# Kernel optimization log

Measured on AMD Instinct MI355X. Metric: run time of the kernel, lower is better.

## Reference

```python
import jax, jax.numpy as jnp
import numpy as np
from jax import lax

B, T, I, O = 32, 4096, 16, 16


def setup_inputs() -> dict:
    key = jax.random.key(0)
    k1, k2, k3, k4 = jax.random.split(key, 4)
    u_in = jax.random.normal(k1, (B, T, I), dtype=jnp.float32)
    # parameters, initialized as in the torch module's __init__
    b_coeff = jax.random.normal(k2, (O, I, 2), dtype=jnp.float32) * 0.01
    rho = jax.random.normal(k3, (O, I, 1), dtype=jnp.float32) * 0.1
    psi = jax.random.normal(k4, (O, I, 1), dtype=jnp.float32) * 0.1
    return {"u_in": u_in, "b_coeff": b_coeff, "rho": rho, "psi": psi}


def _second_order_mimo(u_in, b_coeff, rho, psi):
    # stable parametrization of poles: r = |pole|, theta = angle
    r = jax.nn.sigmoid(rho)[..., 0]            # (O, I)
    theta = np.pi * jax.nn.sigmoid(psi)[..., 0]  # (O, I)
    a1 = -2.0 * r * jnp.cos(theta)             # (O, I)
    a2 = r * r                                  # (O, I)
    b0 = b_coeff[..., 0]                        # (O, I)
    b1 = b_coeff[..., 1]                        # (O, I)

    # FIR (moving-average) part, fully parallel over time:
    # x[b,t,o,i] = b0[o,i]*u[b,t,i] + b1[o,i]*u[b,t-1,i], zero initial condition
    u_prev = jnp.pad(u_in, ((0, 0), (1, 0), (0, 0)))[:, :-1, :]
    x = u_in[:, :, None, :] * b0 + u_prev[:, :, None, :] * b1  # (B, T, O, I)

    # AR (recursive) part: y[t] = x[t] - a1*y[t-1] - a2*y[t-2], per (o,i) pair
    x_t = jnp.moveaxis(x, 1, 0)  # (T, B, O, I)

    def step(carry, xt):
        y1, y2 = carry  # y[t-1], y[t-2], each (B, O, I)
        y = xt - a1 * y1 - a2 * y2
        return (y, y1), y

    y_init = jnp.zeros(x_t.shape[1:], x_t.dtype)
    _, ys = lax.scan(step, (y_init, y_init), x_t)  # (T, B, O, I)

    # sum per-input-channel filter responses -> (B, T, O)
    return jnp.moveaxis(ys.sum(axis=-1), 0, 1)


def reference(u_in, b_coeff, rho, psi):
    return _second_order_mimo(u_in, b_coeff, rho, psi)
```

## Files before the change

kernel.cpp:

```cpp
#include <hip/hip_runtime.h>
#include <math.h>

namespace {

constexpr int B = 32, T = 4096, I = 16, O = 16;

constexpr int C = 128;
constexpr int L = T / C;
constexpr int W = 32;
constexpr int PF = 8;

__device__ __forceinline__ void channel_params(const float* __restrict__ bc,
                                               const float* __restrict__ rho,
                                               const float* __restrict__ psi,
                                               int o, int i,
                                               float& b0, float& b1, float& a1, float& a2) {
    int oi = o * I + i;
    b0 = bc[oi * 2 + 0];
    b1 = bc[oi * 2 + 1];
    float r     = 1.0f / (1.0f + expf(-rho[oi]));
    float theta = 3.14159265358979323846f / (1.0f + expf(-psi[oi]));
    a1 = -2.0f * r * cosf(theta);
    a2 = r * r;
}

template <int NSTEP, int SKIP>
__device__ __forceinline__ void run_chain(const float* __restrict__ up,
        const float b0[4], const float b1[4], const float na1[4], const float na2[4],
        float uprev[4], float* __restrict__ op, bool writer) {
    float y1[4] = {0.f, 0.f, 0.f, 0.f};
    float y2[4] = {0.f, 0.f, 0.f, 0.f};
    float4 buf[PF];
#pragma unroll
    for (int p = 0; p < PF; ++p) buf[p] = *(const float4*)(up + p * I);
#pragma unroll
    for (int t = 0; t < NSTEP; ++t) {
        float4 a = buf[t % PF];
        if (t + PF < NSTEP)
            buf[t % PF] = *(const float4*)(up + (t + PF) * I);
        float uc[4] = {a.x, a.y, a.z, a.w};
        float yv[4];
#pragma unroll
        for (int j = 0; j < 4; ++j) {
            float x = fmaf(b1[j], uprev[j], b0[j] * uc[j]);
            float y = fmaf(na2[j], y2[j], fmaf(na1[j], y1[j], x));
            y2[j] = y1[j]; y1[j] = y; uprev[j] = uc[j];
            yv[j] = y;
        }
        if (t >= SKIP) {
            float s = (yv[0] + yv[1]) + (yv[2] + yv[3]);
            s += __shfl_xor(s, 1);
            s += __shfl_xor(s, 2);
            if (writer) op[(t - SKIP) * O] = s;
        }
    }
}

__global__ __launch_bounds__(256) void mimo_kernel(
        const float* __restrict__ u, const float* __restrict__ bc,
        const float* __restrict__ rho, const float* __restrict__ psi,
        float* __restrict__ out) {
    int g = blockIdx.x * blockDim.x + threadIdx.x;
    int q = g & 3, o = (g >> 2) & 15, b = (g >> 6) & 31, k = g >> 11;
    int i0 = q * 4;

    float b0[4], b1[4], na1[4], na2[4];
#pragma unroll
    for (int j = 0; j < 4; ++j) {
        float B0, B1, A1, A2;
        channel_params(bc, rho, psi, o, i0 + j, B0, B1, A1, A2);
        b0[j] = B0; b1[j] = B1; na1[j] = -A1; na2[j] = -A2;
    }

    int t0 = k * L;
    int start = (k == 0) ? 0 : (t0 - W);
    const float* up = u + ((size_t)b * T + start) * I + i0;

    float uprev[4];
    if (start == 0) {
#pragma unroll
        for (int j = 0; j < 4; ++j) uprev[j] = 0.0f;
    } else {
        float4 r0 = *(const float4*)(up - I);
        uprev[0] = r0.x; uprev[1] = r0.y; uprev[2] = r0.z; uprev[3] = r0.w;
    }

    float* op = out + ((size_t)b * T + t0) * O + o;
    bool writer = (q == 0);

    if (k == 0) run_chain<L, 0>(up, b0, b1, na1, na2, uprev, op, writer);
    else        run_chain<W + L, W>(up, b0, b1, na1, na2, uprev, op, writer);
}

}

extern "C" void kernel_launch(void* const* d_in, const int* in_sizes, int n_in,
                              void* d_out, int out_size, void* d_ws, size_t ws_size,
                              hipStream_t stream) {
    (void)in_sizes; (void)n_in; (void)out_size; (void)d_ws; (void)ws_size;
    const float* u   = (const float*)d_in[0];
    const float* bc  = (const float*)d_in[1];
    const float* rho = (const float*)d_in[2];
    const float* psi = (const float*)d_in[3];
    float* out = (float*)d_out;

    mimo_kernel<<<dim3((B * O * 4 * C) / 256), dim3(256), 0, stream>>>(
        u, bc, rho, psi, out);
}
```

Measured before the change: 81.40 us.

## Split input channels across eight lanes and batch loads per block of steps

Each thread now handles 2 input channels instead of 4, so the grid doubles and the per-thread serial recurrence does half the work per step. Loads become float2 and are issued in blocks of 8 time steps, and the cross-lane reduction and store are grouped per block, using one extra shuffle stage. The warm-up window shrinks from 32 to 24 steps, which cuts redundant recomputation but leaves the truncated-history error decaying over fewer steps. Costs include more threads redundantly loading the same inputs and an extra shuffle per output.

```diff
diff --git a/kernel.cpp b/kernel.cpp
--- a/kernel.cpp
+++ b/kernel.cpp
@@ -5,10 +5,11 @@
 
 constexpr int B = 32, T = 4096, I = 16, O = 16;
 
-constexpr int C = 128;
-constexpr int L = T / C;
-constexpr int W = 32;
-constexpr int PF = 8;
+constexpr int C  = 128;
+constexpr int L  = T / C;
+constexpr int W  = 24;
+constexpr int BS = 8;
+
 
 __device__ __forceinline__ void channel_params(const float* __restrict__ bc,
                                                const float* __restrict__ rho,
@@ -26,32 +27,39 @@
 
 template <int NSTEP, int SKIP>
 __device__ __forceinline__ void run_chain(const float* __restrict__ up,
-        const float b0[4], const float b1[4], const float na1[4], const float na2[4],
-        float uprev[4], float* __restrict__ op, bool writer) {
-    float y1[4] = {0.f, 0.f, 0.f, 0.f};
-    float y2[4] = {0.f, 0.f, 0.f, 0.f};
-    float4 buf[PF];
+        const float b0[2], const float b1[2], const float na1[2], const float na2[2],
+        float up0, float up1, float* __restrict__ op, bool writer) {
+    static_assert(NSTEP % BS == 0 && SKIP % BS == 0, "blocks must align");
+    float y10 = 0.f, y20 = 0.f;
+    float y11 = 0.f, y21 = 0.f;
 #pragma unroll
-    for (int p = 0; p < PF; ++p) buf[p] = *(const float4*)(up + p * I);
+    for (int blk = 0; blk < NSTEP / BS; ++blk) {
+        float2 f[BS];
 #pragma unroll
-    for (int t = 0; t < NSTEP; ++t) {
-        float4 a = buf[t % PF];
-        if (t + PF < NSTEP)
-            buf[t % PF] = *(const float4*)(up + (t + PF) * I);
-        float uc[4] = {a.x, a.y, a.z, a.w};
-        float yv[4];
+        for (int m = 0; m < BS; ++m)
+            f[m] = *(const float2*)(up + (blk * BS + m) * I);
+        float sv[BS];
 #pragma unroll
-        for (int j = 0; j < 4; ++j) {
-            float x = fmaf(b1[j], uprev[j], b0[j] * uc[j]);
-            float y = fmaf(na2[j], y2[j], fmaf(na1[j], y1[j], x));
-            y2[j] = y1[j]; y1[j] = y; uprev[j] = uc[j];
-            yv[j] = y;
+        for (int m = 0; m < BS; ++m) {
+            float uc0 = f[m].x, uc1 = f[m].y;
+            float x0 = fmaf(b1[0], up0, b0[0] * uc0);
+            float y0 = fmaf(na2[0], y20, fmaf(na1[0], y10, x0));
+            y20 = y10; y10 = y0; up0 = uc0;
+            float x1 = fmaf(b1[1], up1, b0[1] * uc1);
+            float y1 = fmaf(na2[1], y21, fmaf(na1[1], y11, x1));
+            y21 = y11; y11 = y1; up1 = uc1;
+            sv[m] = y0 + y1;
         }
-        if (t >= SKIP) {
-            float s = (yv[0] + yv[1]) + (yv[2] + yv[3]);
-            s += __shfl_xor(s, 1);
-            s += __shfl_xor(s, 2);
-            if (writer) op[(t - SKIP) * O] = s;
+        if (blk * BS >= SKIP) {
+            int bt = blk * BS - SKIP;
+#pragma unroll
+            for (int m = 0; m < BS; ++m) {
+                float s = sv[m];
+                s += __shfl_xor(s, 1);
+                s += __shfl_xor(s, 2);
+                s += __shfl_xor(s, 4);
+                if (writer) op[(bt + m) * O] = s;
+            }
         }
     }
 }
@@ -61,12 +69,12 @@
         const float* __restrict__ rho, const float* __restrict__ psi,
         float* __restrict__ out) {
     int g = blockIdx.x * blockDim.x + threadIdx.x;
-    int q = g & 3, o = (g >> 2) & 15, b = (g >> 6) & 31, k = g >> 11;
-    int i0 = q * 4;
+    int p = g & 7, o = (g >> 3) & 15, b = (g >> 7) & 31, k = g >> 12;
+    int i0 = 2 * p;
 
-    float b0[4], b1[4], na1[4], na2[4];
+    float b0[2], b1[2], na1[2], na2[2];
 #pragma unroll
-    for (int j = 0; j < 4; ++j) {
+    for (int j = 0; j < 2; ++j) {
         float B0, B1, A1, A2;
         channel_params(bc, rho, psi, o, i0 + j, B0, B1, A1, A2);
         b0[j] = B0; b1[j] = B1; na1[j] = -A1; na2[j] = -A2;
@@ -76,20 +84,19 @@
     int start = (k == 0) ? 0 : (t0 - W);
     const float* up = u + ((size_t)b * T + start) * I + i0;
 
-    float uprev[4];
-    if (start == 0) {
-#pragma unroll
-        for (int j = 0; j < 4; ++j) uprev[j] = 0.0f;
+    float up0, up1;
+    if (k == 0) {
+        up0 = 0.f; up1 = 0.f;
     } else {
-        float4 r0 = *(const float4*)(up - I);
-        uprev[0] = r0.x; uprev[1] = r0.y; uprev[2] = r0.z; uprev[3] = r0.w;
+        float2 r0 = *(const float2*)(up - I);
+        up0 = r0.x; up1 = r0.y;
     }
 
     float* op = out + ((size_t)b * T + t0) * O + o;
-    bool writer = (q == 0);
+    bool writer = (p == 0);
 
-    if (k == 0) run_chain<L, 0>(up, b0, b1, na1, na2, uprev, op, writer);
-    else        run_chain<W + L, W>(up, b0, b1, na1, na2, uprev, op, writer);
+    if (k == 0) run_chain<L, 0>(up, b0, b1, na1, na2, up0, up1, op, writer);
+    else        run_chain<W + L, W>(up, b0, b1, na1, na2, up0, up1, op, writer);
 }
 
 }
@@ -104,6 +111,6 @@
     const float* psi = (const float*)d_in[3];
     float* out = (float*)d_out;
 
-    mimo_kernel<<<dim3((B * O * 4 * C) / 256), dim3(256), 0, stream>>>(
+    mimo_kernel<<<dim3((B * O * 8 * C) / 256), dim3(256), 0, stream>>>(
         u, bc, rho, psi, out);
 }
```

Result: slower. 83.72 us (+2.8%).
